# Optimization experiments

Measured on AMD Instinct MI355X. Metric: run time of the kernel, lower is better.

## Reference

```python
import jax, jax.numpy as jnp
import numpy as np

N_NODES = 50000
N_EDGES = 800000
D = 128
BATCHSIZE = 64


def setup_inputs() -> dict:
    key = jax.random.key(0)
    k1, k2, k3, k4 = jax.random.split(key, 4)
    x = jax.random.normal(k1, (N_NODES, D), dtype=jnp.float32)
    eps = jnp.zeros((1,), dtype=jnp.float32)
    W_pred = jax.random.normal(k2, (D, D), dtype=jnp.float32) * (1.0 / np.sqrt(D))
    b_pred = jnp.zeros((D,), dtype=jnp.float32)
    edge_index = jax.random.randint(k3, (2, N_EDGES), 0, N_NODES, dtype=jnp.int64)
    batch = jnp.sort(jax.random.randint(k4, (N_NODES,), 0, BATCHSIZE, dtype=jnp.int64))
    return {"x": x, "eps": eps, "W_pred": W_pred, "b_pred": b_pred,
            "edge_index": edge_index, "batch": batch}


def reference(x, eps, W_pred, b_pred, edge_index, batch):
    src, dst = edge_index[0], edge_index[1]
    # spmm: sum of neighbor features for each destination node [N, D]
    agg = jax.ops.segment_sum(x[src], dst, num_segments=N_NODES)
    # eps-weighted self update (apply_func=None, norm=None)
    out = (1.0 + eps) * x + agg
    out = jax.nn.relu(out)  # activation='relu'
    # linear_prediction then per-graph scatter-add pooling
    pooled = out @ W_pred + b_pred  # [N, pooled_features]
    pooled2 = jax.ops.segment_sum(pooled, batch, num_segments=BATCHSIZE)  # [B, pooled]
    return out, pooled2
```

## Files before the change

### kernel.cpp

```cpp
#include <hip/hip_runtime.h>
#include <hip/hip_bf16.h>

#define N_NODES 50000
#define N_EDGES 800000
#define D 128
#define BATCHSIZE 64

#define CHUNK_BITS 7
#define CHUNK 128
#define NBUCKETS 391
#define NBUCKETS_PAD 392
#define CAP 2400
#define BIN_THREADS 256
#define BIN_EPT 8
#define BIN_TILE (BIN_THREADS * BIN_EPT)

__global__ __launch_bounds__(BIN_THREADS) void bin_kernel(
    const int* __restrict__ edge_index,
    int* __restrict__ gcur,
    int* __restrict__ bucket)
{
    __shared__ int cnt[NBUCKETS_PAD];
    __shared__ int gbase[NBUCKETS_PAD];
    __shared__ int lcur[NBUCKETS_PAD];
    int t = threadIdx.x;
    for (int b = t; b < NBUCKETS_PAD; b += BIN_THREADS) { cnt[b] = 0; lcur[b] = 0; }
    __syncthreads();

    int packs[BIN_EPT];
    int bs[BIN_EPT];
    int e0 = blockIdx.x * BIN_TILE + t;
#pragma unroll
    for (int i = 0; i < BIN_EPT; ++i) {
        int e = e0 + i * BIN_THREADS;
        if (e < N_EDGES) {
            int s = edge_index[e];
            int d = edge_index[N_EDGES + e];
            int b = d >> CHUNK_BITS;
            bs[i] = b;
            packs[i] = (s << CHUNK_BITS) | (d & (CHUNK - 1));
            atomicAdd(&cnt[b], 1);
        } else {
            bs[i] = -1;
        }
    }
    __syncthreads();
    for (int b = t; b < NBUCKETS; b += BIN_THREADS) {
        int c = cnt[b];
        gbase[b] = c ? atomicAdd(&gcur[b], c) : 0;
    }
    __syncthreads();
#pragma unroll
    for (int i = 0; i < BIN_EPT; ++i) {
        if (bs[i] >= 0) {
            int p = atomicAdd(&lcur[bs[i]], 1);
            int gpos = gbase[bs[i]] + p;
            if (gpos < CAP) bucket[bs[i] * CAP + gpos] = packs[i];
        }
    }
}

__global__ __launch_bounds__(1024) void gather_sort_kernel(
    const float* __restrict__ x,
    const float* __restrict__ eps,
    const int* __restrict__ batch,
    const int* __restrict__ gcur,
    const int* __restrict__ bucket,
    float* __restrict__ out,
    float* __restrict__ S)
{
    __shared__ int   ebuf[CAP];
    __shared__ int   sorted[CAP];
    __shared__ int   hist[CHUNK];
    __shared__ int   offs[CHUNK + 1];
    __shared__ int   cursor[CHUNK];
    __shared__ float pool[8 * D];

    int c = blockIdx.x;
    int t = threadIdx.x;
    int lane = t & 31;
    int g = t >> 5;

    if (t < CHUNK) hist[t] = 0;
    for (int i = t; i < 8 * D; i += 1024) pool[i] = 0.0f;
    int cnt = gcur[c];
    if (cnt > CAP) cnt = CAP;
    __syncthreads();

    for (int i = t; i < cnt; i += 1024) {
        int p = bucket[c * CAP + i];
        ebuf[i] = p;
        atomicAdd(&hist[p & (CHUNK - 1)], 1);
    }
    __syncthreads();

    if (t < 64) {
        int h0 = hist[2 * t], h1 = hist[2 * t + 1];
        int tot = h0 + h1;
        int incl = tot;
#pragma unroll
        for (int o = 1; o < 64; o <<= 1) {
            int y = __shfl_up(incl, o, 64);
            if (t >= o) incl += y;
        }
        int excl = incl - tot;
        offs[2 * t] = excl;     cursor[2 * t] = excl;
        offs[2 * t + 1] = excl + h0; cursor[2 * t + 1] = excl + h0;
        if (t == 63) offs[CHUNK] = incl;
    }
    __syncthreads();

    for (int i = t; i < cnt; i += 1024) {
        int p = ebuf[i];
        int pos = atomicAdd(&cursor[p & (CHUNK - 1)], 1);
        sorted[pos] = p >> CHUNK_BITS;
    }
    __syncthreads();

    int node0 = c << CHUNK_BITS;
    int base_b = batch[node0];
    float scale = 1.0f + eps[0];
    int dv_cur = -1;
    float4 ps = make_float4(0.f, 0.f, 0.f, 0.f);

#pragma unroll
    for (int k = 0; k < 4; ++k) {
        int d = 4 * g + k;
        int node = node0 + d;
        if (node >= N_NODES) break;
        int start = offs[d], end = offs[d + 1];
        float4 acc = make_float4(0.f, 0.f, 0.f, 0.f);
        int i = start;
        for (; i + 4 <= end; i += 4) {
            int s0 = sorted[i], s1 = sorted[i + 1];
            int s2 = sorted[i + 2], s3 = sorted[i + 3];
            const float4 v0 = *(const float4*)(x + (size_t)s0 * D + lane * 4);
            const float4 v1 = *(const float4*)(x + (size_t)s1 * D + lane * 4);
            const float4 v2 = *(const float4*)(x + (size_t)s2 * D + lane * 4);
            const float4 v3 = *(const float4*)(x + (size_t)s3 * D + lane * 4);
            acc.x += (v0.x + v1.x) + (v2.x + v3.x);
            acc.y += (v0.y + v1.y) + (v2.y + v3.y);
            acc.z += (v0.z + v1.z) + (v2.z + v3.z);
            acc.w += (v0.w + v1.w) + (v2.w + v3.w);
        }
        for (; i < end; ++i) {
            int s0 = sorted[i];
            const float4 v0 = *(const float4*)(x + (size_t)s0 * D + lane * 4);
            acc.x += v0.x; acc.y += v0.y; acc.z += v0.z; acc.w += v0.w;
        }
        const float4 xv = *(const float4*)(x + (size_t)node * D + lane * 4);
        float4 o;
        o.x = fmaxf(fmaf(scale, xv.x, acc.x), 0.0f);
        o.y = fmaxf(fmaf(scale, xv.y, acc.y), 0.0f);
        o.z = fmaxf(fmaf(scale, xv.z, acc.z), 0.0f);
        o.w = fmaxf(fmaf(scale, xv.w, acc.w), 0.0f);
        *(float4*)(out + (size_t)node * D + lane * 4) = o;

        int dv = batch[node] - base_b;
        if (dv != dv_cur) {
            if (dv_cur >= 0) {
                if (dv_cur < 8) {
                    float* pp = &pool[dv_cur * D + lane * 4];
                    atomicAdd(pp + 0, ps.x); atomicAdd(pp + 1, ps.y);
                    atomicAdd(pp + 2, ps.z); atomicAdd(pp + 3, ps.w);
                } else {
                    float* sp = S + (size_t)(base_b + dv_cur) * D + lane * 4;
                    atomicAdd(sp + 0, ps.x); atomicAdd(sp + 1, ps.y);
                    atomicAdd(sp + 2, ps.z); atomicAdd(sp + 3, ps.w);
                }
            }
            ps = make_float4(0.f, 0.f, 0.f, 0.f);
            dv_cur = dv;
        }
        ps.x += o.x; ps.y += o.y; ps.z += o.z; ps.w += o.w;
    }
    if (dv_cur >= 0) {
        if (dv_cur < 8) {
            float* pp = &pool[dv_cur * D + lane * 4];
            atomicAdd(pp + 0, ps.x); atomicAdd(pp + 1, ps.y);
            atomicAdd(pp + 2, ps.z); atomicAdd(pp + 3, ps.w);
        } else {
            float* sp = S + (size_t)(base_b + dv_cur) * D + lane * 4;
            atomicAdd(sp + 0, ps.x); atomicAdd(sp + 1, ps.y);
            atomicAdd(sp + 2, ps.z); atomicAdd(sp + 3, ps.w);
        }
    }
    __syncthreads();

    int lastnode = node0 + CHUNK - 1;
    if (lastnode >= N_NODES) lastnode = N_NODES - 1;
    int used = batch[lastnode] - base_b + 1;
    if (used > 8) used = 8;
    for (int i = t; i < used * D; i += 1024) {
        atomicAdd(&S[(size_t)base_b * D + i], pool[i]);
    }
}

__device__ inline int lower_bound_dev(const int* __restrict__ a, int n, int key) {
    int lo = 0, hi = n;
    while (lo < hi) {
        int mid = (lo + hi) >> 1;
        if (a[mid] < key) lo = mid + 1; else hi = mid;
    }
    return lo;
}

__global__ void pool_gemm_kernel(const float* __restrict__ S,
                                 const int* __restrict__ batch,
                                 const float* __restrict__ W,
                                 const float* __restrict__ b_pred,
                                 float* __restrict__ pooled2) {
    int b = blockIdx.x;
    int j = threadIdx.x;
    int lo = lower_bound_dev(batch, N_NODES, b);
    int hi = lower_bound_dev(batch, N_NODES, b + 1);
    float acc = (float)(hi - lo) * b_pred[j];
    const float* srow = S + (size_t)b * D;
#pragma unroll 8
    for (int k = 0; k < D; ++k) {
        acc = fmaf(srow[k], W[(size_t)k * D + j], acc);
    }
    pooled2[(size_t)b * D + j] = acc;
}


__global__ void edge_scatter_kernel(const float* __restrict__ x,
                                    const int* __restrict__ edge_index,
                                    float* __restrict__ agg) {
    int tid = blockIdx.x * blockDim.x + threadIdx.x;
    int lane = tid & 31;
    int e = tid >> 5;
    if (e >= N_EDGES) return;
    int src = edge_index[e];
    int dst = edge_index[N_EDGES + e];
    const float4 v = *(const float4*)(x + (size_t)src * D + lane * 4);
    float* dp = agg + (size_t)dst * D + lane * 4;
    atomicAdd(dp + 0, v.x);
    atomicAdd(dp + 1, v.y);
    atomicAdd(dp + 2, v.z);
    atomicAdd(dp + 3, v.w);
}

__global__ void finalize_kernel(const float* __restrict__ x,
                                const float* __restrict__ eps,
                                const int* __restrict__ batch,
                                float* __restrict__ out,
                                float* __restrict__ Sf,
                                float* __restrict__ counts) {
    int tid = blockIdx.x * blockDim.x + threadIdx.x;
    int lane = tid & 31;
    int node = tid >> 5;
    if (node >= N_NODES) return;
    float scale = 1.0f + eps[0];
    const float4 xv = *(const float4*)(x + (size_t)node * D + lane * 4);
    float4 av = *(float4*)(out + (size_t)node * D + lane * 4);
    float4 o;
    o.x = fmaxf(fmaf(scale, xv.x, av.x), 0.0f);
    o.y = fmaxf(fmaf(scale, xv.y, av.y), 0.0f);
    o.z = fmaxf(fmaf(scale, xv.z, av.z), 0.0f);
    o.w = fmaxf(fmaf(scale, xv.w, av.w), 0.0f);
    *(float4*)(out + (size_t)node * D + lane * 4) = o;
    int b = batch[node];
    float* sp = Sf + (size_t)b * D + lane * 4;
    atomicAdd(sp + 0, o.x);
    atomicAdd(sp + 1, o.y);
    atomicAdd(sp + 2, o.z);
    atomicAdd(sp + 3, o.w);
    if (lane == 0) atomicAdd(counts + b, 1.0f);
}

__global__ void pool_gemm_fallback_kernel(const float* __restrict__ Sf,
                                          const float* __restrict__ counts,
                                          const float* __restrict__ W,
                                          const float* __restrict__ b_pred,
                                          float* __restrict__ pooled2) {
    int b = blockIdx.x;
    int j = threadIdx.x;
    float acc = counts[b] * b_pred[j];
    const float* srow = Sf + (size_t)b * D;
#pragma unroll 8
    for (int k = 0; k < D; ++k) {
        acc = fmaf(srow[k], W[(size_t)k * D + j], acc);
    }
    pooled2[(size_t)b * D + j] = acc;
}

extern "C" void kernel_launch(void* const* d_in, const int* in_sizes, int n_in,
                              void* d_out, int out_size, void* d_ws, size_t ws_size,
                              hipStream_t stream) {
    const float* x      = (const float*)d_in[0];
    const float* eps    = (const float*)d_in[1];
    const float* W_pred = (const float*)d_in[2];
    const float* b_pred = (const float*)d_in[3];
    const int*   eidx   = (const int*)d_in[4];
    const int*   batch  = (const int*)d_in[5];

    float* out     = (float*)d_out;
    float* pooled2 = (float*)d_out + (size_t)N_NODES * D;

    const size_t need = (size_t)(NBUCKETS_PAD + BATCHSIZE * D + (size_t)NBUCKETS * CAP) * 4;

    if (ws_size >= need) {
        int*   gcur   = (int*)d_ws;
        float* S      = (float*)d_ws + NBUCKETS_PAD;
        int*   bucket = (int*)d_ws + NBUCKETS_PAD + BATCHSIZE * D;

        hipMemsetAsync(d_ws, 0, (size_t)(NBUCKETS_PAD + BATCHSIZE * D) * 4, stream);

        int bin_blocks = (N_EDGES + BIN_TILE - 1) / BIN_TILE;
        bin_kernel<<<bin_blocks, BIN_THREADS, 0, stream>>>(eidx, gcur, bucket);
        gather_sort_kernel<<<NBUCKETS, 1024, 0, stream>>>(x, eps, batch, gcur, bucket, out, S);
        pool_gemm_kernel<<<BATCHSIZE, D, 0, stream>>>(S, batch, W_pred, b_pred, pooled2);
    } else {
        float* Sf      = (float*)d_ws;
        float* countsf = (float*)d_ws + BATCHSIZE * D;
        hipMemsetAsync(out, 0, (size_t)N_NODES * D * sizeof(float), stream);
        hipMemsetAsync(d_ws, 0, (BATCHSIZE * D + BATCHSIZE) * sizeof(float), stream);
        {
            long long total = (long long)N_EDGES * 32;
            int blocks = (int)((total + 255) / 256);
            edge_scatter_kernel<<<blocks, 256, 0, stream>>>(x, eidx, out);
        }
        {
            long long total = (long long)N_NODES * 32;
            int blocks = (int)((total + 255) / 256);
            finalize_kernel<<<blocks, 256, 0, stream>>>(x, eps, batch, out, Sf, countsf);
        }
        pool_gemm_fallback_kernel<<<BATCHSIZE, D, 0, stream>>>(Sf, countsf, W_pred, b_pred, pooled2);
    }
}
```

Before: 172.7 us.

## Gather neighbor features from a bf16 copy of x and locally sort edge bins

Adds a conversion kernel that writes a bf16 copy of x into workspace, and the gather kernel then reads neighbor rows as bf16, halving the bytes fetched by the random gather. The binning kernel is rewritten to use large tiles that are counting-sorted in shared memory before being written per bucket, so global writes are grouped by bucket instead of scattered. The cost is an extra full pass over x for conversion, reduced accuracy in the aggregated sum, and per-thread serial copy loops in the bin writeout.

```diff
diff --git a/kernel.cpp b/kernel.cpp
--- a/kernel.cpp
+++ b/kernel.cpp
@@ -10,58 +10,109 @@
 #define CHUNK 128
 #define NBUCKETS 391
 #define NBUCKETS_PAD 392
+#define CNT_PAD 448
 #define CAP 2400
-#define BIN_THREADS 256
-#define BIN_EPT 8
-#define BIN_TILE (BIN_THREADS * BIN_EPT)
-
-__global__ __launch_bounds__(BIN_THREADS) void bin_kernel(
+
+#define BIN2_THREADS 512
+#define BIN2_TILE 16384
+#define BIN2_BLOCKS ((N_EDGES + BIN2_TILE - 1) / BIN2_TILE)
+
+__device__ inline unsigned short f2bf(float f) {
+    union { float f; unsigned u; } c; c.f = f;
+    unsigned u = c.u;
+    return (unsigned short)((u + 0x7fffu + ((u >> 16) & 1u)) >> 16);
+}
+
+__device__ inline float4 bf4_to_f4(uint2 u) {
+    union { unsigned u; float f; } a, b, c, d;
+    a.u = u.x << 16; b.u = u.x & 0xffff0000u;
+    c.u = u.y << 16; d.u = u.y & 0xffff0000u;
+    float4 r; r.x = a.f; r.y = b.f; r.z = c.f; r.w = d.f;
+    return r;
+}
+
+__global__ __launch_bounds__(256) void convert_kernel(const float* __restrict__ x,
+                                                      unsigned short* __restrict__ xb) {
+    int i = (blockIdx.x * 256 + threadIdx.x) * 4;
+    if (i >= N_NODES * D) return;
+    float4 v = *(const float4*)(x + i);
+    unsigned short o0 = f2bf(v.x), o1 = f2bf(v.y), o2 = f2bf(v.z), o3 = f2bf(v.w);
+    uint2 pk;
+    pk.x = (unsigned)o0 | ((unsigned)o1 << 16);
+    pk.y = (unsigned)o2 | ((unsigned)o3 << 16);
+    *(uint2*)(xb + i) = pk;
+}
+
+__global__ __launch_bounds__(BIN2_THREADS) void bin2_kernel(
     const int* __restrict__ edge_index,
     int* __restrict__ gcur,
     int* __restrict__ bucket)
 {
-    __shared__ int cnt[NBUCKETS_PAD];
+    __shared__ int cnt[CNT_PAD];
+    __shared__ int loffs[CNT_PAD];
     __shared__ int gbase[NBUCKETS_PAD];
-    __shared__ int lcur[NBUCKETS_PAD];
+    __shared__ int cursor[NBUCKETS_PAD];
+    __shared__ int sortbuf[BIN2_TILE];
+
     int t = threadIdx.x;
-    for (int b = t; b < NBUCKETS_PAD; b += BIN_THREADS) { cnt[b] = 0; lcur[b] = 0; }
-    __syncthreads();
-
-    int packs[BIN_EPT];
-    int bs[BIN_EPT];
-    int e0 = blockIdx.x * BIN_TILE + t;
+    for (int b = t; b < CNT_PAD; b += BIN2_THREADS) cnt[b] = 0;
+    __syncthreads();
+
+    int base = blockIdx.x * BIN2_TILE;
+    int lim = N_EDGES - base; if (lim > BIN2_TILE) lim = BIN2_TILE;
+
+    for (int i = t; i < lim; i += BIN2_THREADS) {
+        int d = edge_index[N_EDGES + base + i];
+        atomicAdd(&cnt[d >> CHUNK_BITS], 1);
+    }
+    __syncthreads();
+
+    if (t < 64) {
+        int l[7]; int s = 0;
 #pragma unroll
-    for (int i = 0; i < BIN_EPT; ++i) {
-        int e = e0 + i * BIN_THREADS;
-        if (e < N_EDGES) {
-            int s = edge_index[e];
-            int d = edge_index[N_EDGES + e];
-            int b = d >> CHUNK_BITS;
-            bs[i] = b;
-            packs[i] = (s << CHUNK_BITS) | (d & (CHUNK - 1));
-            atomicAdd(&cnt[b], 1);
-        } else {
-            bs[i] = -1;
-        }
-    }
-    __syncthreads();
-    for (int b = t; b < NBUCKETS; b += BIN_THREADS) {
+        for (int j = 0; j < 7; ++j) { l[j] = s; s += cnt[t * 7 + j]; }
+        int incl = s;
+#pragma unroll
+        for (int o = 1; o < 64; o <<= 1) {
+            int y = __shfl_up(incl, o, 64);
+            if (t >= o) incl += y;
+        }
+        int excl = incl - s;
+#pragma unroll
+        for (int j = 0; j < 7; ++j) loffs[t * 7 + j] = excl + l[j];
+    }
+    __syncthreads();
+
+    for (int b = t; b < NBUCKETS; b += BIN2_THREADS) {
         int c = cnt[b];
         gbase[b] = c ? atomicAdd(&gcur[b], c) : 0;
-    }
-    __syncthreads();
-#pragma unroll
-    for (int i = 0; i < BIN_EPT; ++i) {
-        if (bs[i] >= 0) {
-            int p = atomicAdd(&lcur[bs[i]], 1);
-            int gpos = gbase[bs[i]] + p;
-            if (gpos < CAP) bucket[bs[i] * CAP + gpos] = packs[i];
-        }
-    }
-}
-
+        cursor[b] = loffs[b];
+    }
+    __syncthreads();
+
+    for (int i = t; i < lim; i += BIN2_THREADS) {
+        int s = edge_index[base + i];
+        int d = edge_index[N_EDGES + base + i];
+        int b = d >> CHUNK_BITS;
+        int pos = atomicAdd(&cursor[b], 1);
+        sortbuf[pos] = (s << CHUNK_BITS) | (d & (CHUNK - 1));
+    }
+    __syncthreads();
+
+    for (int b = t; b < NBUCKETS; b += BIN2_THREADS) {
+        int c = cnt[b], lo = loffs[b], gb = gbase[b];
+        int* dstp = bucket + (size_t)b * CAP;
+        for (int j = 0; j < c; ++j) {
+            int gp = gb + j;
+            if (gp < CAP) dstp[gp] = sortbuf[lo + j];
+        }
+    }
+}
+
+template<bool BF16>
 __global__ __launch_bounds__(1024) void gather_sort_kernel(
     const float* __restrict__ x,
+    const unsigned short* __restrict__ xb,
     const float* __restrict__ eps,
     const int* __restrict__ batch,
     const int* __restrict__ gcur,
@@ -88,7 +139,7 @@
     __syncthreads();
 
     for (int i = t; i < cnt; i += 1024) {
-        int p = bucket[c * CAP + i];
+        int p = bucket[(size_t)c * CAP + i];
         ebuf[i] = p;
         atomicAdd(&hist[p & (CHUNK - 1)], 1);
     }
@@ -104,7 +155,7 @@
             if (t >= o) incl += y;
         }
         int excl = incl - tot;
-        offs[2 * t] = excl;     cursor[2 * t] = excl;
+        offs[2 * t] = excl;          cursor[2 * t] = excl;
         offs[2 * t + 1] = excl + h0; cursor[2 * t + 1] = excl + h0;
         if (t == 63) offs[CHUNK] = incl;
     }
@@ -131,22 +182,43 @@
         int start = offs[d], end = offs[d + 1];
         float4 acc = make_float4(0.f, 0.f, 0.f, 0.f);
         int i = start;
-        for (; i + 4 <= end; i += 4) {
-            int s0 = sorted[i], s1 = sorted[i + 1];
-            int s2 = sorted[i + 2], s3 = sorted[i + 3];
-            const float4 v0 = *(const float4*)(x + (size_t)s0 * D + lane * 4);
-            const float4 v1 = *(const float4*)(x + (size_t)s1 * D + lane * 4);
-            const float4 v2 = *(const float4*)(x + (size_t)s2 * D + lane * 4);
-            const float4 v3 = *(const float4*)(x + (size_t)s3 * D + lane * 4);
-            acc.x += (v0.x + v1.x) + (v2.x + v3.x);
-            acc.y += (v0.y + v1.y) + (v2.y + v3.y);
-            acc.z += (v0.z + v1.z) + (v2.z + v3.z);
-            acc.w += (v0.w + v1.w) + (v2.w + v3.w);
-        }
-        for (; i < end; ++i) {
-            int s0 = sorted[i];
-            const float4 v0 = *(const float4*)(x + (size_t)s0 * D + lane * 4);
-            acc.x += v0.x; acc.y += v0.y; acc.z += v0.z; acc.w += v0.w;
+        if (BF16) {
+            for (; i + 4 <= end; i += 4) {
+                int s0 = sorted[i], s1 = sorted[i + 1];
+                int s2 = sorted[i + 2], s3 = sorted[i + 3];
+                uint2 u0 = *(const uint2*)(xb + (size_t)s0 * D + lane * 4);
+                uint2 u1 = *(const uint2*)(xb + (size_t)s1 * D + lane * 4);
+                uint2 u2 = *(const uint2*)(xb + (size_t)s2 * D + lane * 4);
+                uint2 u3 = *(const uint2*)(xb + (size_t)s3 * D + lane * 4);
+                float4 v0 = bf4_to_f4(u0), v1 = bf4_to_f4(u1);
+                float4 v2 = bf4_to_f4(u2), v3 = bf4_to_f4(u3);
+                acc.x += (v0.x + v1.x) + (v2.x + v3.x);
+                acc.y += (v0.y + v1.y) + (v2.y + v3.y);
+                acc.z += (v0.z + v1.z) + (v2.z + v3.z);
+                acc.w += (v0.w + v1.w) + (v2.w + v3.w);
+            }
+            for (; i < end; ++i) {
+                uint2 u0 = *(const uint2*)(xb + (size_t)sorted[i] * D + lane * 4);
+                float4 v0 = bf4_to_f4(u0);
+                acc.x += v0.x; acc.y += v0.y; acc.z += v0.z; acc.w += v0.w;
+            }
+        } else {
+            for (; i + 4 <= end; i += 4) {
+                int s0 = sorted[i], s1 = sorted[i + 1];
+                int s2 = sorted[i + 2], s3 = sorted[i + 3];
+                const float4 v0 = *(const float4*)(x + (size_t)s0 * D + lane * 4);
+                const float4 v1 = *(const float4*)(x + (size_t)s1 * D + lane * 4);
+                const float4 v2 = *(const float4*)(x + (size_t)s2 * D + lane * 4);
+                const float4 v3 = *(const float4*)(x + (size_t)s3 * D + lane * 4);
+                acc.x += (v0.x + v1.x) + (v2.x + v3.x);
+                acc.y += (v0.y + v1.y) + (v2.y + v3.y);
+                acc.z += (v0.z + v1.z) + (v2.z + v3.z);
+                acc.w += (v0.w + v1.w) + (v2.w + v3.w);
+            }
+            for (; i < end; ++i) {
+                const float4 v0 = *(const float4*)(x + (size_t)sorted[i] * D + lane * 4);
+                acc.x += v0.x; acc.y += v0.y; acc.z += v0.z; acc.w += v0.w;
+            }
         }
         const float4 xv = *(const float4*)(x + (size_t)node * D + lane * 4);
         float4 o;
@@ -298,18 +370,27 @@
     float* out     = (float*)d_out;
     float* pooled2 = (float*)d_out + (size_t)N_NODES * D;
 
-    const size_t need = (size_t)(NBUCKETS_PAD + BATCHSIZE * D + (size_t)NBUCKETS * CAP) * 4;
-
-    if (ws_size >= need) {
+    const size_t base_ints = (size_t)NBUCKETS_PAD + BATCHSIZE * D + (size_t)NBUCKETS * CAP;
+    const size_t need_mid  = base_ints * 4;
+    const size_t need_full = (base_ints + (size_t)N_NODES * D / 2) * 4;
+
+    if (ws_size >= need_mid) {
         int*   gcur   = (int*)d_ws;
         float* S      = (float*)d_ws + NBUCKETS_PAD;
         int*   bucket = (int*)d_ws + NBUCKETS_PAD + BATCHSIZE * D;
+        unsigned short* xb = (unsigned short*)((int*)d_ws + base_ints);
 
         hipMemsetAsync(d_ws, 0, (size_t)(NBUCKETS_PAD + BATCHSIZE * D) * 4, stream);
 
-        int bin_blocks = (N_EDGES + BIN_TILE - 1) / BIN_TILE;
-        bin_kernel<<<bin_blocks, BIN_THREADS, 0, stream>>>(eidx, gcur, bucket);
-        gather_sort_kernel<<<NBUCKETS, 1024, 0, stream>>>(x, eps, batch, gcur, bucket, out, S);
+        bin2_kernel<<<BIN2_BLOCKS, BIN2_THREADS, 0, stream>>>(eidx, gcur, bucket);
+        if (ws_size >= need_full) {
+            convert_kernel<<<(N_NODES * D / 4 + 255) / 256, 256, 0, stream>>>(x, xb);
+            gather_sort_kernel<true><<<NBUCKETS, 1024, 0, stream>>>(
+                x, xb, eps, batch, gcur, bucket, out, S);
+        } else {
+            gather_sort_kernel<false><<<NBUCKETS, 1024, 0, stream>>>(
+                x, (const unsigned short*)nullptr, eps, batch, gcur, bucket, out, S);
+        }
         pool_gemm_kernel<<<BATCHSIZE, D, 0, stream>>>(S, batch, W_pred, b_pred, pooled2);
     } else {
         float* Sf      = (float*)d_ws;
```

Result: slower. 178.8 us (+3.5%).
